# Performance work log

Measured on AMD Instinct MI355X. Metric: run time of the kernel, lower is better.

Reference implementation:

```python
import jax, jax.numpy as jnp
import numpy as np

B, C, H, W = 64, 3, 512, 512
WEIGHT = 1.0


def _high_freq_mask(h, w):
    m = np.ones((h, w), dtype=np.float32)
    ch, cw = h // 2, w // 2
    m[ch - h // 8:ch + h // 8, cw - w // 8:cw + w // 8] = 0.0
    return jnp.asarray(m), float(m.sum())


def setup_inputs() -> dict:
    key = jax.random.key(0)
    k1, k2 = jax.random.split(key)
    # images in [-1, 1]
    generated = jax.random.uniform(k1, (B, C, H, W), dtype=jnp.float32, minval=-1.0, maxval=1.0)
    target = jax.random.uniform(k2, (B, C, H, W), dtype=jnp.float32, minval=-1.0, maxval=1.0)
    return {"generated": generated, "target": target}


def _to_gray01(x):
    # (B,3,H,W) in [-1,1] -> (B,H,W) grayscale in [0,1]
    g = x[:, 0] * 0.299 + x[:, 1] * 0.587 + x[:, 2] * 0.114
    return (g + 1.0) * 0.5


def _high_freq_psd(gray):
    # gray: (B,H,W) float32
    h, w = gray.shape[-2:]
    mask, count = _high_freq_mask(h, w)
    fft = jnp.fft.fftshift(jnp.fft.fft2(gray), axes=(-2, -1))  # (B,H,W) complex64
    psd = jnp.real(fft) ** 2 + jnp.imag(fft) ** 2
    psd_log = jnp.log10(psd + 1e-10)
    # mean over high-frequency (masked) region; count is static
    return jnp.sum(psd_log * mask, axis=(-2, -1)) / count  # (B,)


def reference(generated, target):
    psd_gen = _high_freq_psd(_to_gray01(generated))
    psd_tgt = _high_freq_psd(_to_gray01(target))
    loss = jnp.mean(jnp.abs(psd_gen - psd_tgt))  # F.l1_loss
    return WEIGHT * loss
```

## Files before the change

### kernel.cpp

```cpp
#include <hip/hip_runtime.h>
#include <math.h>

#ifndef M_PI
#define M_PI 3.14159265358979323846
#endif


__device__ __forceinline__ float2 cmulf(float2 a, float2 b) {
    return make_float2(fmaf(a.x, b.x, -(a.y * b.y)), fmaf(a.x, b.y, a.y * b.x));
}
__device__ __forceinline__ float2 caddf(float2 a, float2 b){ return make_float2(a.x+b.x, a.y+b.y); }
__device__ __forceinline__ float2 csubf(float2 a, float2 b){ return make_float2(a.x-b.x, a.y-b.y); }

__device__ __forceinline__ void lds_order() {
    __builtin_amdgcn_sched_barrier(0);
}

__device__ __forceinline__ void dft8(float2 v[8]) {
    const float S = 0.70710678118654752440f;
    float2 a0=caddf(v[0],v[4]), a1=caddf(v[1],v[5]), a2=caddf(v[2],v[6]), a3=caddf(v[3],v[7]);
    float2 b0=csubf(v[0],v[4]);
    float2 t1=csubf(v[1],v[5]);
    float2 t2=csubf(v[2],v[6]);
    float2 t3=csubf(v[3],v[7]);
    float2 b1=make_float2(S*(t1.x+t1.y), S*(t1.y-t1.x));
    float2 b2=make_float2(t2.y, -t2.x);
    float2 b3=make_float2(S*(t3.y-t3.x), -S*(t3.x+t3.y));
    float2 c0=caddf(a0,a2), c1=caddf(a1,a3), c2=csubf(a0,a2);
    float2 u3=csubf(a1,a3); float2 c3=make_float2(u3.y,-u3.x);
    float2 d0=caddf(b0,b2), d1=caddf(b1,b3), d2=csubf(b0,b2);
    float2 w3=csubf(b1,b3); float2 d3=make_float2(w3.y,-w3.x);
    v[0]=caddf(c0,c1); v[4]=csubf(c0,c1);
    v[2]=caddf(c2,c3); v[6]=csubf(c2,c3);
    v[1]=caddf(d0,d1); v[5]=csubf(d0,d1);
    v[3]=caddf(d2,d3); v[7]=csubf(d2,d3);
}

__device__ __forceinline__ void twapply(float2 v[8], float2 w) {
    const float2 w2 = cmulf(w,  w);
    const float2 w3 = cmulf(w2, w);
    const float2 w4 = cmulf(w2, w2);
    const float2 w5 = cmulf(w2, w3);
    const float2 w6 = cmulf(w3, w3);
    const float2 w7 = cmulf(w4, w3);
    v[1] = cmulf(v[1], w);
    v[2] = cmulf(v[2], w2);
    v[3] = cmulf(v[3], w3);
    v[4] = cmulf(v[4], w4);
    v[5] = cmulf(v[5], w5);
    v[6] = cmulf(v[6], w6);
    v[7] = cmulf(v[7], w7);
}

__device__ __forceinline__ void fft512_reg(float2 v[8], float2* __restrict__ W,
                                           const float2* __restrict__ twg, int lane) {
    dft8(v);
    twapply(v, twg[lane]);
#pragma unroll
    for (int c = 0; c < 8; ++c) W[(c<<6) + ((lane + 2*c)&63)] = v[c];
    lds_order();
    {
        const int c = lane>>3, p = lane&7, base = c<<6, off = p + 2*c;
#pragma unroll
        for (int bb = 0; bb < 8; ++bb) v[bb] = W[base + (((bb<<3) + off)&63)];
    }
    lds_order();
    dft8(v);
    twapply(v, twg[(lane&7)<<3]);
    {
        const int c = lane>>3, p = lane&7, base = c<<6, r2 = 2*c;
#pragma unroll
        for (int d = 0; d < 8; ++d) W[base + (((d<<3) + (p^d) + r2)&63)] = v[d];
    }
    lds_order();
    {
        const int c = lane>>3, d = lane&7, base = c<<6, off = (d<<3) + 2*c;
#pragma unroll
        for (int p = 0; p < 8; ++p) v[p] = W[base + ((off + (p^d))&63)];
    }
    lds_order();
    dft8(v);
}

__global__ void twiddle_kernel(float2* __restrict__ tw) {
    const int k = threadIdx.x;
    const double ang = -2.0 * M_PI * (double)k / 512.0;
    tw[k] = make_float2((float)cos(ang), (float)sin(ang));
}

__global__ __launch_bounds__(512, 4)
void row_fft_kernel(const float* __restrict__ gen, const float* __restrict__ tgt,
                    const float2* __restrict__ twg, float2* __restrict__ scratch,
                    int b0) {
    __shared__ float2 SBUF[8 * 512];
    const int tid = threadIdx.x, wave = tid>>6, lane = tid&63;
    const int img = blockIdx.x>>6, rg = blockIdx.x&63;
    const int b = b0 + img, r = (rg<<3) + wave;

    const size_t rowoff = ((size_t)b * 3 * 512 + r) * 512;
    const float* gR = gen + rowoff; const float* gG = gR + 262144; const float* gB = gG + 262144;
    const float* tR = tgt + rowoff; const float* tG = tR + 262144; const float* tB = tG + 262144;

    float2 v[8];
#pragma unroll
    for (int a = 0; a < 8; ++a) {
        const int idx = (a<<6) + lane;
        const float gg = fmaf(0.299f, gR[idx], fmaf(0.587f, gG[idx], fmaf(0.114f, gB[idx], 1.0f))) * 0.5f;
        const float tt = fmaf(0.299f, tR[idx], fmaf(0.587f, tG[idx], fmaf(0.114f, tB[idx], 1.0f))) * 0.5f;
        v[a] = make_float2(gg, tt);
    }

    float2* W = SBUF + (wave<<9);
    fft512_reg(v, W, twg, lane);

#pragma unroll
    for (int e = 0; e < 8; ++e) {
        const int col = (e<<6) + lane;
        W[(col + (wave<<3)) & 511] = v[e];
    }
    __syncthreads();

    const size_t obase = (size_t)img << 18;
    const int r0 = rg<<3;
#pragma unroll
    for (int it = 0; it < 8; ++it) {
        const int col = (tid>>3) + (it<<6);
        const int j = tid&7;
        scratch[obase + ((size_t)col<<9) + r0 + j] = SBUF[(j<<9) + ((col + (j<<3)) & 511)];
    }
}

__device__ __forceinline__ void accum_psd(float2 F1, float2 F2, double& sg, double& st) {
    const float ar = 0.5f*(F1.x + F2.x), ai = 0.5f*(F1.y - F2.y);
    const float br = 0.5f*(F1.y + F2.y), bi = 0.5f*(F2.x - F1.x);
    const float pg = fmaf(ar, ar, ai*ai) + 1e-10f;
    const float pt = fmaf(br, br, bi*bi) + 1e-10f;
    sg += (double)log10f(pg);
    st += (double)log10f(pt);
}

__global__ __launch_bounds__(256, 4)
void col_fft_reduce_kernel(const float2* __restrict__ scratch,
                           const float2* __restrict__ twg,
                           double2* __restrict__ partial, int b0) {
    __shared__ float2 SBUF[4 * 512];
    const int tid = threadIdx.x, wave = tid>>6, lane = tid&63;
    const int gw = (blockIdx.x<<2) + wave;
    const int img = gw>>8, t = gw&255;
    const int b = b0 + img;
    const int kxA = t;
    const int kxB = (t == 0) ? 256 : 512 - t;
    const int colA = ((kxA>>6)<<6) + ((kxA&7)<<3) + ((kxA>>3)&7);
    const int colB = ((kxB>>6)<<6) + ((kxB&7)<<3) + ((kxB>>3)&7);
    float2* W = SBUF + (wave<<9);

    const float2* srcA = scratch + ((size_t)img<<18) + ((size_t)colA<<9);
    const float2* srcB = scratch + ((size_t)img<<18) + ((size_t)colB<<9);
    float2 va[8], vb[8];
#pragma unroll
    for (int a = 0; a < 8; ++a) va[a] = srcA[(a<<6) + lane];
#pragma unroll
    for (int a = 0; a < 8; ++a) vb[a] = srcB[(a<<6) + lane];

    fft512_reg(va, W, twg, lane);

    const int cc = lane>>3, dd = lane&7;
    const int kyb = cc + (dd<<3);

#pragma unroll
    for (int e = 0; e < 8; ++e) W[kyb + (e<<6)] = va[e];
    lds_order();
    float2 aRev[8];
#pragma unroll
    for (int e = 0; e < 8; ++e) aRev[e] = W[(512 - (kyb + (e<<6))) & 511];
    lds_order();

    fft512_reg(vb, W, twg, lane);

#pragma unroll
    for (int e = 0; e < 8; ++e) W[kyb + (e<<6)] = vb[e];
    lds_order();
    float2 bRev[8];
#pragma unroll
    for (int e = 0; e < 8; ++e) bRev[e] = W[(512 - (kyb + (e<<6))) & 511];
    lds_order();

    const bool kxinA = (t < 64);
    const bool kxinB = (t >= 1 && t <= 64);

    double sg = 0.0, st = 0.0;
    if (t == 0) {
#pragma unroll
        for (int e = 0; e < 8; ++e) {
            if (!(kxinA && (e == 0 || e == 7))) accum_psd(va[e], aRev[e], sg, st);
            accum_psd(vb[e], bRev[e], sg, st);
        }
    } else {
#pragma unroll
        for (int e = 0; e < 8; ++e) {
            if (!(kxinA && (e == 0 || e == 7))) accum_psd(va[e], bRev[e], sg, st);
            if (!(kxinB && (e == 0 || e == 7))) accum_psd(vb[e], aRev[e], sg, st);
        }
    }
#pragma unroll
    for (int off = 32; off; off >>= 1) {
        sg += __shfl_down(sg, off);
        st += __shfl_down(st, off);
    }
    if (lane == 0) partial[((size_t)b<<8) + t] = make_double2(sg, st);
}

__global__ __launch_bounds__(256)
void reduce_partial_kernel(const double2* __restrict__ partial,
                           double* __restrict__ accum) {
    __shared__ double2 red[4];
    const int img = blockIdx.x, tid = threadIdx.x, wave = tid>>6, lane = tid&63;
    const double2 p = partial[((size_t)img<<8) + tid];
    double sg = p.x, st = p.y;
#pragma unroll
    for (int off = 32; off; off >>= 1) {
        sg += __shfl_down(sg, off);
        st += __shfl_down(st, off);
    }
    if (lane == 0) red[wave] = make_double2(sg, st);
    __syncthreads();
    if (tid == 0) {
        double SG = 0.0, ST = 0.0;
#pragma unroll
        for (int w = 0; w < 4; ++w) { SG += red[w].x; ST += red[w].y; }
        accum[img] = SG;
        accum[64 + img] = ST;
    }
}

__global__ void finalize_kernel(const double* __restrict__ accum,
                                float* __restrict__ out) {
    const int lane = threadIdx.x;
    double d = fabs(accum[lane] - accum[64 + lane]) * (1.0 / 245760.0);
#pragma unroll
    for (int off = 32; off; off >>= 1) d += __shfl_down(d, off);
    if (lane == 0) out[0] = (float)(d * (1.0 / 64.0));
}

extern "C" void kernel_launch(void* const* d_in, const int* in_sizes, int n_in,
                              void* d_out, int out_size, void* d_ws, size_t ws_size,
                              hipStream_t stream) {
    (void)in_sizes; (void)n_in; (void)out_size;
    const float* gen = (const float*)d_in[0];
    const float* tgt = (const float*)d_in[1];
    float*   out     = (float*)d_out;
    float2*  tw      = (float2*)d_ws;
    double*  accum   = (double*)((char*)d_ws + 2048);
    double2* partial = (double2*)((char*)d_ws + 4096);
    float2*  scratch = (float2*)((char*)d_ws + 266240);

    const size_t per_img = (size_t)512 * 512 * sizeof(float2);
    const size_t avail = (ws_size > 266240) ? (ws_size - 266240) : 0;
    int chunk = 64;
    while (chunk > 1 && (size_t)chunk * per_img > avail) chunk >>= 1;

    twiddle_kernel<<<1, 256, 0, stream>>>(tw);
    for (int b0 = 0; b0 < 64; b0 += chunk) {
        row_fft_kernel<<<dim3(chunk * 64), dim3(512), 0, stream>>>(gen, tgt, tw, scratch, b0);
        col_fft_reduce_kernel<<<dim3(chunk * 64), dim3(256), 0, stream>>>(scratch, tw, partial, b0);
    }
    reduce_partial_kernel<<<dim3(64), dim3(256), 0, stream>>>(partial, accum);
    finalize_kernel<<<1, 64, 0, stream>>>(accum, out);
}
```

Measured before the change: 499.2 us.

## Process 16 rows per row-FFT block and store transposed scratch as float4

Each row-FFT block now handles two rows per wave (16 rows per block), doubling shared memory. The transposed write to scratch emits 16-byte float4 stores covering two adjacent rows instead of 8-byte stores, which improves write coalescing. A new LDS rotation (65 per row) is meant to avoid bank conflicts. The cost is higher register and LDS use per block, which may lower occupancy.

```diff
diff --git a/kernel.cpp b/kernel.cpp
--- a/kernel.cpp
+++ b/kernel.cpp
@@ -92,41 +92,64 @@
 void row_fft_kernel(const float* __restrict__ gen, const float* __restrict__ tgt,
                     const float2* __restrict__ twg, float2* __restrict__ scratch,
                     int b0) {
-    __shared__ float2 SBUF[8 * 512];
+    __shared__ float2 SBUF[16 * 512];
     const int tid = threadIdx.x, wave = tid>>6, lane = tid&63;
-    const int img = blockIdx.x>>6, rg = blockIdx.x&63;
-    const int b = b0 + img, r = (rg<<3) + wave;
-
-    const size_t rowoff = ((size_t)b * 3 * 512 + r) * 512;
-    const float* gR = gen + rowoff; const float* gG = gR + 262144; const float* gB = gG + 262144;
-    const float* tR = tgt + rowoff; const float* tG = tR + 262144; const float* tB = tG + 262144;
-
-    float2 v[8];
+    const int img = blockIdx.x>>5, rb = blockIdx.x&31;
+    const int b = b0 + img, r0 = rb<<4;
+    const int rA = r0 + wave, rB = r0 + 8 + wave;
+
+    const size_t baseA = ((size_t)b * 3 * 512 + rA) * 512;
+    const size_t baseB = ((size_t)b * 3 * 512 + rB) * 512;
+    const float* gRA = gen + baseA; const float* gGA = gRA + 262144; const float* gBA = gGA + 262144;
+    const float* tRA = tgt + baseA; const float* tGA = tRA + 262144; const float* tBA = tGA + 262144;
+    const float* gRB = gen + baseB; const float* gGB = gRB + 262144; const float* gBB = gGB + 262144;
+    const float* tRB = tgt + baseB; const float* tGB = tRB + 262144; const float* tBB = tGB + 262144;
+
+    float2 va[8], vb[8];
 #pragma unroll
     for (int a = 0; a < 8; ++a) {
         const int idx = (a<<6) + lane;
-        const float gg = fmaf(0.299f, gR[idx], fmaf(0.587f, gG[idx], fmaf(0.114f, gB[idx], 1.0f))) * 0.5f;
-        const float tt = fmaf(0.299f, tR[idx], fmaf(0.587f, tG[idx], fmaf(0.114f, tB[idx], 1.0f))) * 0.5f;
-        v[a] = make_float2(gg, tt);
-    }
-
-    float2* W = SBUF + (wave<<9);
-    fft512_reg(v, W, twg, lane);
-
-#pragma unroll
-    for (int e = 0; e < 8; ++e) {
-        const int col = (e<<6) + lane;
-        W[(col + (wave<<3)) & 511] = v[e];
+        const float gg = fmaf(0.299f, gRA[idx], fmaf(0.587f, gGA[idx], fmaf(0.114f, gBA[idx], 1.0f))) * 0.5f;
+        const float tt = fmaf(0.299f, tRA[idx], fmaf(0.587f, tGA[idx], fmaf(0.114f, tBA[idx], 1.0f))) * 0.5f;
+        va[a] = make_float2(gg, tt);
+    }
+#pragma unroll
+    for (int a = 0; a < 8; ++a) {
+        const int idx = (a<<6) + lane;
+        const float gg = fmaf(0.299f, gRB[idx], fmaf(0.587f, gGB[idx], fmaf(0.114f, gBB[idx], 1.0f))) * 0.5f;
+        const float tt = fmaf(0.299f, tRB[idx], fmaf(0.587f, tGB[idx], fmaf(0.114f, tBB[idx], 1.0f))) * 0.5f;
+        vb[a] = make_float2(gg, tt);
+    }
+
+    float2* WA = SBUF + (wave<<9);
+    float2* WB = SBUF + ((8+wave)<<9);
+
+    fft512_reg(va, WA, twg, lane);
+    {
+        const int rot = 65 * wave;
+#pragma unroll
+        for (int e = 0; e < 8; ++e) WA[(((e<<6) + lane) + rot) & 511] = va[e];
+    }
+    fft512_reg(vb, WB, twg, lane);
+    {
+        const int rot = 65 * (8 + wave);
+#pragma unroll
+        for (int e = 0; e < 8; ++e) WB[(((e<<6) + lane) + rot) & 511] = vb[e];
     }
     __syncthreads();
 
     const size_t obase = (size_t)img << 18;
-    const int r0 = rg<<3;
+    const int cg = tid>>3, u = tid&7, j0 = u<<1;
+    const int rotl0 = 65*j0, rotl1 = 65*(j0+1);
+    float2* s0 = SBUF + (j0<<9);
+    float2* s1 = SBUF + ((j0+1)<<9);
 #pragma unroll
     for (int it = 0; it < 8; ++it) {
-        const int col = (tid>>3) + (it<<6);
-        const int j = tid&7;
-        scratch[obase + ((size_t)col<<9) + r0 + j] = SBUF[(j<<9) + ((col + (j<<3)) & 511)];
+        const int col = cg + (it<<6);
+        const float2 x0 = s0[(col + rotl0) & 511];
+        const float2 x1 = s1[(col + rotl1) & 511];
+        float4 st = make_float4(x0.x, x0.y, x1.x, x1.y);
+        *reinterpret_cast<float4*>(&scratch[obase + ((size_t)col<<9) + r0 + j0]) = st;
     }
 }
 
@@ -261,7 +284,7 @@
 
     twiddle_kernel<<<1, 256, 0, stream>>>(tw);
     for (int b0 = 0; b0 < 64; b0 += chunk) {
-        row_fft_kernel<<<dim3(chunk * 64), dim3(512), 0, stream>>>(gen, tgt, tw, scratch, b0);
+        row_fft_kernel<<<dim3(chunk * 32), dim3(512), 0, stream>>>(gen, tgt, tw, scratch, b0);
         col_fft_reduce_kernel<<<dim3(chunk * 64), dim3(256), 0, stream>>>(scratch, tw, partial, b0);
     }
     reduce_partial_kernel<<<dim3(64), dim3(256), 0, stream>>>(partial, accum);
```

New measurement: 527.3 us. 5.6% more time.
